# Kernel tuning notes

Measured on AMD Instinct MI355X. Metric: run time of the kernel, lower is better.

The kernel has to match this reference:

```python
import jax, jax.numpy as jnp
import numpy as np

B, S, H, T = 64, 512, 768, 400


def setup_inputs() -> dict:
    key = jax.random.key(0)
    k1, k2 = jax.random.split(key)
    hidden = jax.random.normal(k1, (B, S, H), dtype=jnp.float32)
    # word_ids: non-decreasing piece->word map per sample, like HF tokenizer word_ids()
    word_ids = jnp.sort(jax.random.randint(k2, (B, S), 0, T), axis=-1).astype(jnp.int32)
    return {"hidden": hidden, "word_ids": word_ids, "num_tokens": T}


def reference(hidden, word_ids, num_tokens):
    # Ragged segment mean-pool: pool subword pieces into per-word reps.
    # hidden: [B, S, H] float; word_ids: [B, S] int in [0, num_tokens)
    b, s, h = hidden.shape
    # Flatten (sample, word) into one global segment id: sample*T + word
    seg = (jnp.arange(b, dtype=word_ids.dtype)[:, None] * num_tokens + word_ids).reshape(-1)
    sums = jax.ops.segment_sum(hidden.reshape(b * s, h), seg, num_segments=b * num_tokens)
    counts = jax.ops.segment_sum(jnp.ones((b * s,), hidden.dtype), seg, num_segments=b * num_tokens)
    # Words with zero pieces -> sum 0 / 1 = 0, matching torch.zeros fallback
    pooled = sums / jnp.maximum(counts, 1.0)[:, None]
    return pooled.reshape(b, num_tokens, h)
```

## Files before the change

### kernel.cpp

```cpp
#include <hip/hip_runtime.h>


#define BB 64
#define SS 512
#define HH 768
#define TT 400

__global__ __launch_bounds__(64) void bert_lattice_pool_kernel(
    const float* __restrict__ hidden,
    const int* __restrict__ word_ids,
    float* __restrict__ out)
{
    const int bt = blockIdx.x;
    const int b  = bt / TT;
    const int t  = bt - b * TT;

    const int* wrow = word_ids + b * SS;

    int lo = 0, hi = SS;
    while (lo < hi) {
        int mid = (lo + hi) >> 1;
        if (wrow[mid] < t) lo = mid + 1; else hi = mid;
    }
    const int start = lo;
    hi = SS;
    while (lo < hi) {
        int mid = (lo + hi) >> 1;
        if (wrow[mid] <= t) lo = mid + 1; else hi = mid;
    }
    const int end   = lo;
    const int count = end - start;

    const int lane = threadIdx.x;

    float4 acc0 = make_float4(0.f, 0.f, 0.f, 0.f);
    float4 acc1 = make_float4(0.f, 0.f, 0.f, 0.f);
    float4 acc2 = make_float4(0.f, 0.f, 0.f, 0.f);

    for (int s = start; s < end; ++s) {
        const float4* p =
            reinterpret_cast<const float4*>(hidden + ((size_t)b * SS + s) * HH);
        float4 v0 = p[lane];
        float4 v1 = p[lane + 64];
        float4 v2 = p[lane + 128];
        acc0.x += v0.x; acc0.y += v0.y; acc0.z += v0.z; acc0.w += v0.w;
        acc1.x += v1.x; acc1.y += v1.y; acc1.z += v1.z; acc1.w += v1.w;
        acc2.x += v2.x; acc2.y += v2.y; acc2.z += v2.z; acc2.w += v2.w;
    }

    const float inv = 1.0f / (float)(count > 0 ? count : 1);

    float4* o = reinterpret_cast<float4*>(out + ((size_t)b * TT + t) * HH);
    float4 r0 = make_float4(acc0.x * inv, acc0.y * inv, acc0.z * inv, acc0.w * inv);
    float4 r1 = make_float4(acc1.x * inv, acc1.y * inv, acc1.z * inv, acc1.w * inv);
    float4 r2 = make_float4(acc2.x * inv, acc2.y * inv, acc2.z * inv, acc2.w * inv);
    o[lane]       = r0;
    o[lane + 64]  = r1;
    o[lane + 128] = r2;
}

extern "C" void kernel_launch(void* const* d_in, const int* in_sizes, int n_in,
                              void* d_out, int out_size, void* d_ws, size_t ws_size,
                              hipStream_t stream) {
    (void)in_sizes; (void)n_in; (void)d_ws; (void)ws_size; (void)out_size;
    const float* hidden   = (const float*)d_in[0];
    const int*   word_ids = (const int*)d_in[1];
    float*       out      = (float*)d_out;

    dim3 grid(BB * TT);
    dim3 block(64);
    bert_lattice_pool_kernel<<<grid, block, 0, stream>>>(hidden, word_ids, out);
}
```

Measured before the change: 176.6 us.

## Process chunks of 16 words per block with shared-memory segment boundaries

After: 179.5 us. Within noise of the previous version (+1.6%).

```diff
diff --git a/kernel.cpp b/kernel.cpp
--- a/kernel.cpp
+++ b/kernel.cpp
@@ -5,58 +5,75 @@
 #define SS 512
 #define HH 768
 #define TT 400
+#define TCHUNK 16
+#define NCHUNK (TT / TCHUNK)
 
-__global__ __launch_bounds__(64) void bert_lattice_pool_kernel(
+__global__ __launch_bounds__(256) void bert_lattice_pool_kernel(
     const float* __restrict__ hidden,
     const int* __restrict__ word_ids,
     float* __restrict__ out)
 {
-    const int bt = blockIdx.x;
-    const int b  = bt / TT;
-    const int t  = bt - b * TT;
+    __shared__ int wid[SS];
+    __shared__ int sstart[TCHUNK];
+    __shared__ int send[TCHUNK];
 
-    const int* wrow = word_ids + b * SS;
+    const int blk = blockIdx.x;
+    const int b   = blk / NCHUNK;
+    const int t0  = (blk - b * NCHUNK) * TCHUNK;
 
-    int lo = 0, hi = SS;
-    while (lo < hi) {
-        int mid = (lo + hi) >> 1;
-        if (wrow[mid] < t) lo = mid + 1; else hi = mid;
+    const int tid = threadIdx.x;
+
+    {
+        const int2* src = reinterpret_cast<const int2*>(word_ids + b * SS);
+        reinterpret_cast<int2*>(wid)[tid] = src[tid];
     }
-    const int start = lo;
-    hi = SS;
-    while (lo < hi) {
-        int mid = (lo + hi) >> 1;
-        if (wrow[mid] <= t) lo = mid + 1; else hi = mid;
+    if (tid < TCHUNK) { sstart[tid] = 0; send[tid] = 0; }
+    __syncthreads();
+
+    #pragma unroll
+    for (int k = 0; k < SS / 256; ++k) {
+        const int s   = tid + k * 256;
+        const int w   = wid[s];
+        const int rel = w - t0;
+        if (rel >= 0 && rel < TCHUNK) {
+            if (s == 0      || wid[s - 1] != w) sstart[rel] = s;
+            if (s == SS - 1 || wid[s + 1] != w) send[rel]   = s + 1;
+        }
     }
-    const int end   = lo;
-    const int count = end - start;
+    __syncthreads();
 
-    const int lane = threadIdx.x;
+    const int wave = tid >> 6;
+    const int lane = tid & 63;
 
-    float4 acc0 = make_float4(0.f, 0.f, 0.f, 0.f);
-    float4 acc1 = make_float4(0.f, 0.f, 0.f, 0.f);
-    float4 acc2 = make_float4(0.f, 0.f, 0.f, 0.f);
+    #pragma unroll
+    for (int i = 0; i < TCHUNK / 4; ++i) {
+        const int trel  = wave * (TCHUNK / 4) + i;
+        const int start = sstart[trel];
+        const int end   = send[trel];
+        const int count = end - start;
 
-    for (int s = start; s < end; ++s) {
-        const float4* p =
-            reinterpret_cast<const float4*>(hidden + ((size_t)b * SS + s) * HH);
-        float4 v0 = p[lane];
-        float4 v1 = p[lane + 64];
-        float4 v2 = p[lane + 128];
-        acc0.x += v0.x; acc0.y += v0.y; acc0.z += v0.z; acc0.w += v0.w;
-        acc1.x += v1.x; acc1.y += v1.y; acc1.z += v1.z; acc1.w += v1.w;
-        acc2.x += v2.x; acc2.y += v2.y; acc2.z += v2.z; acc2.w += v2.w;
+        float4 acc0 = make_float4(0.f, 0.f, 0.f, 0.f);
+        float4 acc1 = make_float4(0.f, 0.f, 0.f, 0.f);
+        float4 acc2 = make_float4(0.f, 0.f, 0.f, 0.f);
+
+        for (int s = start; s < end; ++s) {
+            const float4* p =
+                reinterpret_cast<const float4*>(hidden + ((size_t)b * SS + s) * HH);
+            float4 v0 = p[lane];
+            float4 v1 = p[lane + 64];
+            float4 v2 = p[lane + 128];
+            acc0.x += v0.x; acc0.y += v0.y; acc0.z += v0.z; acc0.w += v0.w;
+            acc1.x += v1.x; acc1.y += v1.y; acc1.z += v1.z; acc1.w += v1.w;
+            acc2.x += v2.x; acc2.y += v2.y; acc2.z += v2.z; acc2.w += v2.w;
+        }
+
+        const float inv = 1.0f / (float)(count > 0 ? count : 1);
+
+        float4* o = reinterpret_cast<float4*>(out + ((size_t)b * TT + t0 + trel) * HH);
+        o[lane]       = make_float4(acc0.x * inv, acc0.y * inv, acc0.z * inv, acc0.w * inv);
+        o[lane + 64]  = make_float4(acc1.x * inv, acc1.y * inv, acc1.z * inv, acc1.w * inv);
+        o[lane + 128] = make_float4(acc2.x * inv, acc2.y * inv, acc2.z * inv, acc2.w * inv);
     }
-
-    const float inv = 1.0f / (float)(count > 0 ? count : 1);
-
-    float4* o = reinterpret_cast<float4*>(out + ((size_t)b * TT + t) * HH);
-    float4 r0 = make_float4(acc0.x * inv, acc0.y * inv, acc0.z * inv, acc0.w * inv);
-    float4 r1 = make_float4(acc1.x * inv, acc1.y * inv, acc1.z * inv, acc1.w * inv);
-    float4 r2 = make_float4(acc2.x * inv, acc2.y * inv, acc2.z * inv, acc2.w * inv);
-    o[lane]       = r0;
-    o[lane + 64]  = r1;
-    o[lane + 128] = r2;
 }
 
 extern "C" void kernel_launch(void* const* d_in, const int* in_sizes, int n_in,
@@ -67,7 +84,7 @@
     const int*   word_ids = (const int*)d_in[1];
     float*       out      = (float*)d_out;
 
-    dim3 grid(BB * TT);
-    dim3 block(64);
+    dim3 grid(BB * NCHUNK);
+    dim3 block(256);
     bert_lattice_pool_kernel<<<grid, block, 0, stream>>>(hidden, word_ids, out);
 }
```
